# Optimization experiments

Hardware: AMD Instinct MI355X
Metric: run time of the kernel (lower is better)

## Reference

```python
import jax, jax.numpy as jnp
import numpy as np

K = 5        # kernel_size
F0 = 3       # features[0]
F1 = 3       # features[1]
N = 2097152  # ring length (number of sites)
NOISE = 0.01

# triple_product[a,b,c] = cross(tetra[a], tetra[b]) @ tetra[c], shape (4,4,4)
_t = np.array([[0.0, 0.0, 1.0],
               [(8/9)**0.5, 0.0, -1/3],
               [-(2/9)**0.5, (2/3)**0.5, -1/3],
               [-(2/9)**0.5, -(2/3)**0.5, -1/3]], dtype=np.float64)
_cross = np.cross(_t[:, None, :], _t[None, :, :])          # (4,4,3)
TRIPLE_PRODUCT = jnp.asarray(np.einsum('abd,cd->abc', _cross, _t), dtype=jnp.float32)


def setup_inputs() -> dict:
    key = jax.random.key(0)
    ks = jax.random.split(key, 5)
    x = jax.random.randint(ks[0], (N,), 0, 4, dtype=jnp.int32)
    input_kernel_dot = NOISE * jax.random.normal(ks[1], (F0, K), jnp.float32)
    input_kernel_triple = NOISE * jax.random.normal(ks[2], (F0, K, K), jnp.float32)
    kernel_0 = jax.random.normal(ks[3], (K, 2 * F0, F1), jnp.float32) / np.float32(np.sqrt(K * 2 * F0))
    bias_0 = jnp.zeros((1, F1), jnp.float32)
    dense_w = jax.random.normal(ks[4], (F1, 1), jnp.float32) / np.float32(np.sqrt(F1))
    return {"x": x, "input_kernel_dot": input_kernel_dot,
            "input_kernel_triple": input_kernel_triple, "kernel_0": kernel_0,
            "bias_0": bias_0, "dense_w": dense_w}


def reference(x, input_kernel_dot, input_kernel_triple, kernel_0, bias_0, dense_w):
    n = x.shape[0]
    i = jnp.arange(n)
    # ring neighbors x[(i+1)..(i+K) mod N], shape (N, K)
    nbr = (i[:, None] + jnp.arange(1, K + 1)[None, :]) % n
    xn = x[nbr]
    # dot channel: +/-1 same-spin indicator contracted with (F0,K) kernel
    same = 2.0 * (x[:, None] == xn).astype(jnp.float32) - 1.0      # (N,K)
    y_dot = jnp.einsum('fk,nk->nf', input_kernel_dot, same)        # (N,F0)
    # triple channel: antisymmetrized kernel against triple-product lookup
    anti = input_kernel_triple - jnp.swapaxes(input_kernel_triple, 1, 2)   # (F0,K,K)
    tpl = TRIPLE_PRODUCT[x[:, None, None], xn[:, :, None], xn[:, None, :]]  # (N,K,K)
    y_triple = jnp.einsum('fjk,njk->nf', anti, tpl)                # (N,F0)
    y = jax.nn.elu(jnp.concatenate([y_dot, y_triple], axis=1))     # (N,2*F0)
    # circular conv layer: roll(y, i)[:K][j] == y[(j - i) % N]
    conv_idx = (jnp.arange(K)[None, :] - i[:, None]) % n           # (N,K)
    y = jnp.einsum('jcf,njc->nf', kernel_0, y[conv_idx]) + bias_0  # (N,F1)
    y = jax.nn.elu(y)
    y = jnp.mean(y, axis=0)                                        # (F1,)
    return (y @ dense_w).ravel()[0]
```

## Files before the change

kernel.cpp:

```cpp
#include <hip/hip_runtime.h>
#include <math.h>

#define NSITES 2097152
#define NMASK  (NSITES - 1)

__device__ __forceinline__ float elu1(float v) {
    return v > 0.0f ? v : __expf(v) - 1.0f;
}

__device__ __forceinline__ float tp_val(int a, int b, int c) {
    if (a == b || b == c || a == c) return 0.0f;
    int inv = (a > b) + (a > c) + (b > c);
    int d   = 6 - a - b - c;
    float base = (d & 1) ? 0.76980035891950105f : -0.76980035891950105f;
    return (inv & 1) ? -base : base;
}

__global__ __launch_bounds__(1024) void su2_fused_kernel(
    const int*   __restrict__ x,
    const float* __restrict__ kdot,
    const float* __restrict__ ktri,
    const float* __restrict__ k0,
    const float* __restrict__ bias,
    const float* __restrict__ dw,
    float*       __restrict__ out)
{
    __shared__ float4       s4[4096];
    __shared__ float2       s2[4096];
    __shared__ unsigned int hc[1024];
    __shared__ float        tp[64];
    __shared__ float        red[16];

    const int tid = threadIdx.x;

    const int m0 = (blockIdx.x * 1024 + tid) * 8;
    const int4 xa = *reinterpret_cast<const int4*>(x + m0);
    const int4 xb = *reinterpret_cast<const int4*>(x + m0 + 4);

    int4 e0, e1, e2;
    if (tid >= 1022) {
        e0 = *reinterpret_cast<const int4*>(x + ((m0 + 8)  & NMASK));
        e1 = *reinterpret_cast<const int4*>(x + ((m0 + 12) & NMASK));
        e2 = *reinterpret_cast<const int4*>(x + ((m0 + 16) & NMASK));
    }

    if (tid < 64) tp[tid] = tp_val(tid >> 4, (tid >> 2) & 3, tid & 3);

    unsigned int half =
        (unsigned)xa.x | ((unsigned)xa.y << 2) | ((unsigned)xa.z << 4) | ((unsigned)xa.w << 6) |
        ((unsigned)xb.x << 8) | ((unsigned)xb.y << 10) | ((unsigned)xb.z << 12) | ((unsigned)xb.w << 14);
    hc[tid] = half;

    float kd[3][5];
    #pragma unroll
    for (int f = 0; f < 3; ++f)
        #pragma unroll
        for (int k = 0; k < 5; ++k) kd[f][k] = kdot[f * 5 + k];

    float an[3][10];
    #pragma unroll
    for (int f = 0; f < 3; ++f) {
        int p = 0;
        #pragma unroll
        for (int j = 0; j < 5; ++j)
            #pragma unroll
            for (int k = j + 1; k < 5; ++k) {
                an[f][p] = 2.0f * (ktri[f * 25 + j * 5 + k] - ktri[f * 25 + k * 5 + j]);
                ++p;
            }
    }
    __syncthreads();

    {
        const int a = tid & 3;
        int nb[4];
        #pragma unroll
        for (int k = 0; k < 4; ++k) nb[k] = (tid >> (2 + 2 * k)) & 3;

        float yd0 = 0.f, yd1 = 0.f, yd2 = 0.f;
        #pragma unroll
        for (int k = 0; k < 4; ++k) {
            const float sm = (a == nb[k]) ? 1.0f : -1.0f;
            yd0 = fmaf(kd[0][k], sm, yd0);
            yd1 = fmaf(kd[1][k], sm, yd1);
            yd2 = fmaf(kd[2][k], sm, yd2);
        }

        float ft0 = 0.f, ft1 = 0.f, ft2 = 0.f;
        {
            const int pj[6] = {0, 0, 0, 1, 1, 2};
            const int pk[6] = {1, 2, 3, 2, 3, 3};
            const int pp[6] = {0, 1, 2, 4, 5, 7};
            #pragma unroll
            for (int q = 0; q < 6; ++q) {
                const float t = tp[(a << 4) + (nb[pj[q]] << 2) + nb[pk[q]]];
                ft0 = fmaf(an[0][pp[q]], t, ft0);
                ft1 = fmaf(an[1][pp[q]], t, ft1);
                ft2 = fmaf(an[2][pp[q]], t, ft2);
            }
        }

        #pragma unroll
        for (int i = 0; i < 4; ++i) {
            const int code = tid + 1024 * i;
            const float sm4 = (a == i) ? 1.0f : -1.0f;
            const float d0v = fmaf(kd[0][4], sm4, yd0);
            const float d1v = fmaf(kd[1][4], sm4, yd1);
            const float d2v = fmaf(kd[2][4], sm4, yd2);

            float t0 = ft0, t1 = ft1, t2 = ft2;
            const int p4[4] = {3, 6, 8, 9};
            #pragma unroll
            for (int j = 0; j < 4; ++j) {
                const float t = tp[(a << 4) + (nb[j] << 2) + i];
                t0 = fmaf(an[0][p4[j]], t, t0);
                t1 = fmaf(an[1][p4[j]], t, t1);
                t2 = fmaf(an[2][p4[j]], t, t2);
            }

            s4[code] = make_float4(elu1(d0v), elu1(d1v), elu1(d2v), elu1(t0));
            s2[code] = make_float2(elu1(t1), elu1(t2));
        }
    }
    __syncthreads();

    unsigned long long code;
    if (tid < 1022) {
        code = (unsigned long long)half
             | ((unsigned long long)hc[tid + 1] << 16)
             | ((unsigned long long)(hc[tid + 2] & 3u) << 32);
    } else {
        code = (unsigned long long)half
             | ((unsigned long long)(unsigned)e0.x << 16) | ((unsigned long long)(unsigned)e0.y << 18)
             | ((unsigned long long)(unsigned)e0.z << 20) | ((unsigned long long)(unsigned)e0.w << 22)
             | ((unsigned long long)(unsigned)e1.x << 24) | ((unsigned long long)(unsigned)e1.y << 26)
             | ((unsigned long long)(unsigned)e1.z << 28) | ((unsigned long long)(unsigned)e1.w << 30)
             | ((unsigned long long)(unsigned)e2.x << 32);
    }

    const float b0 = bias[0], b1 = bias[1], b2 = bias[2];
    float acc[8][3];
    #pragma unroll
    for (int o = 0; o < 8; ++o) { acc[o][0] = b0; acc[o][1] = b1; acc[o][2] = b2; }

    #pragma unroll
    for (int i = 0; i < 12; ++i) {
        const int idx = (int)((code >> (2 * i)) & 0xFFFull);
        const float4 a4 = s4[idx];
        const float2 a2 = s2[idx];
        const float y[6] = { a4.x, a4.y, a4.z, a4.w, a2.x, a2.y };
        #pragma unroll
        for (int j = 0; j < 5; ++j) {
            const int o = i - j;
            if (o >= 0 && o < 8) {
                #pragma unroll
                for (int c = 0; c < 6; ++c) {
                    const int kb = (j * 6 + c) * 3;
                    acc[o][0] = fmaf(k0[kb + 0], y[c], acc[o][0]);
                    acc[o][1] = fmaf(k0[kb + 1], y[c], acc[o][1]);
                    acc[o][2] = fmaf(k0[kb + 2], y[c], acc[o][2]);
                }
            }
        }
    }

    const float d0 = dw[0], d1 = dw[1], d2 = dw[2];
    float partial = 0.0f;
    #pragma unroll
    for (int o = 0; o < 8; ++o)
        partial += elu1(acc[o][0]) * d0 + elu1(acc[o][1]) * d1 + elu1(acc[o][2]) * d2;

    #pragma unroll
    for (int off = 32; off > 0; off >>= 1)
        partial += __shfl_down(partial, off, 64);

    if ((tid & 63) == 0) red[tid >> 6] = partial;
    __syncthreads();

    if (tid == 0) {
        float s = 0.0f;
        #pragma unroll
        for (int w = 0; w < 16; ++w) s += red[w];
        atomicAdd(out, s * (1.0f / (float)NSITES));
    }
}

extern "C" void kernel_launch(void* const* d_in, const int* in_sizes, int n_in,
                              void* d_out, int out_size, void* d_ws, size_t ws_size,
                              hipStream_t stream) {
    const int*   x    = (const int*)  d_in[0];
    const float* kdot = (const float*)d_in[1];
    const float* ktri = (const float*)d_in[2];
    const float* k0   = (const float*)d_in[3];
    const float* bias = (const float*)d_in[4];
    const float* dw   = (const float*)d_in[5];
    float* out = (float*)d_out;

    su2_fused_kernel<<<NSITES / 8192, 1024, 0, stream>>>(x, kdot, ktri, k0, bias, dw, out);
}
```

Measured before the change: 82.98 us.

## Store conv lookup table in fp16 and use packed fdot2 for convolution

The per-code first-layer activations in shared memory move from fp32 float4+float2 to three fp16x2 arrays. The conv weights are pre-packed into fp16 pairs in registers. The inner convolution uses v_dot2 (fdot2) with fp32 accumulation, halving the FMA count and the LDS traffic per lookup. This trades accuracy of activations and weights for less arithmetic and bandwidth, and it adds register pressure from holding the packed weights.

```diff
diff --git a/kernel.cpp b/kernel.cpp
--- a/kernel.cpp
+++ b/kernel.cpp
@@ -3,6 +3,8 @@
 
 #define NSITES 2097152
 #define NMASK  (NSITES - 1)
+
+typedef _Float16 half2_t __attribute__((ext_vector_type(2)));
 
 __device__ __forceinline__ float elu1(float v) {
     return v > 0.0f ? v : __expf(v) - 1.0f;
@@ -25,8 +27,9 @@
     const float* __restrict__ dw,
     float*       __restrict__ out)
 {
-    __shared__ float4       s4[4096];
-    __shared__ float2       s2[4096];
+    __shared__ half2_t      t01[4096];
+    __shared__ half2_t      t23[4096];
+    __shared__ half2_t      t45[4096];
     __shared__ unsigned int hc[1024];
     __shared__ float        tp[64];
     __shared__ float        red[16];
@@ -69,6 +72,16 @@
                 ++p;
             }
     }
+
+    half2_t w01[5][3], w23[5][3], w45[5][3];
+    #pragma unroll
+    for (int j = 0; j < 5; ++j)
+        #pragma unroll
+        for (int f = 0; f < 3; ++f) {
+            w01[j][f] = half2_t{(_Float16)k0[(j * 6 + 0) * 3 + f], (_Float16)k0[(j * 6 + 1) * 3 + f]};
+            w23[j][f] = half2_t{(_Float16)k0[(j * 6 + 2) * 3 + f], (_Float16)k0[(j * 6 + 3) * 3 + f]};
+            w45[j][f] = half2_t{(_Float16)k0[(j * 6 + 4) * 3 + f], (_Float16)k0[(j * 6 + 5) * 3 + f]};
+        }
     __syncthreads();
 
     {
@@ -118,8 +131,9 @@
                 t2 = fmaf(an[2][p4[j]], t, t2);
             }
 
-            s4[code] = make_float4(elu1(d0v), elu1(d1v), elu1(d2v), elu1(t0));
-            s2[code] = make_float2(elu1(t1), elu1(t2));
+            t01[code] = half2_t{(_Float16)elu1(d0v), (_Float16)elu1(d1v)};
+            t23[code] = half2_t{(_Float16)elu1(d2v), (_Float16)elu1(t0)};
+            t45[code] = half2_t{(_Float16)elu1(t1),  (_Float16)elu1(t2)};
         }
     }
     __syncthreads();
@@ -146,19 +160,20 @@
     #pragma unroll
     for (int i = 0; i < 12; ++i) {
         const int idx = (int)((code >> (2 * i)) & 0xFFFull);
-        const float4 a4 = s4[idx];
-        const float2 a2 = s2[idx];
-        const float y[6] = { a4.x, a4.y, a4.z, a4.w, a2.x, a2.y };
+        const half2_t v01 = t01[idx];
+        const half2_t v23 = t23[idx];
+        const half2_t v45 = t45[idx];
         #pragma unroll
         for (int j = 0; j < 5; ++j) {
             const int o = i - j;
             if (o >= 0 && o < 8) {
                 #pragma unroll
-                for (int c = 0; c < 6; ++c) {
-                    const int kb = (j * 6 + c) * 3;
-                    acc[o][0] = fmaf(k0[kb + 0], y[c], acc[o][0]);
-                    acc[o][1] = fmaf(k0[kb + 1], y[c], acc[o][1]);
-                    acc[o][2] = fmaf(k0[kb + 2], y[c], acc[o][2]);
+                for (int f = 0; f < 3; ++f) {
+                    float a = acc[o][f];
+                    a = __builtin_amdgcn_fdot2(v01, w01[j][f], a, false);
+                    a = __builtin_amdgcn_fdot2(v23, w23[j][f], a, false);
+                    a = __builtin_amdgcn_fdot2(v45, w45[j][f], a, false);
+                    acc[o][f] = a;
                 }
             }
         }
```

Result: faster. 80.93 us (median of 2 runs) (-2.5%).
